# Kernel tuning notes

Measured on AMD Instinct MI355X. Metric: run time of the kernel, lower is better.

Reference implementation:

```python
import jax, jax.numpy as jnp
import numpy as np

DIM = 1024
HEADS = 16
HEAD_DIM = DIM // HEADS
MLP_HID = 4 * DIM
EPS = 1e-5


def layer_norm(x, g, b):
    mu = jnp.mean(x, axis=-1, keepdims=True)
    var = jnp.mean(jnp.square(x - mu), axis=-1, keepdims=True)
    return (x - mu) * jax.lax.rsqrt(var + EPS) * g + b


def setup_inputs() -> dict:
    key = jax.random.key(0)
    ks = jax.random.split(key, 8)
    s_in = 1.0 / np.sqrt(DIM)
    s_hid = 1.0 / np.sqrt(MLP_HID)
    return {
        "x": jax.random.normal(ks[0], (4, 2048, DIM), dtype=jnp.float32),
        "qkv_w": jax.random.uniform(ks[1], (3 * DIM, DIM), jnp.float32, -s_in, s_in),
        "proj_w": jax.random.uniform(ks[2], (DIM, DIM), jnp.float32, -s_in, s_in),
        "proj_b": jnp.zeros((DIM,), jnp.float32),
        "ln1_g": jnp.ones((DIM,), jnp.float32),
        "ln1_b": jnp.zeros((DIM,), jnp.float32),
        "w1": jax.random.uniform(ks[3], (MLP_HID, DIM), jnp.float32, -s_in, s_in),
        "b1": jnp.zeros((MLP_HID,), jnp.float32),
        "prelu_a": jnp.asarray(0.25, jnp.float32),
        "w2": jax.random.uniform(ks[4], (DIM, MLP_HID), jnp.float32, -s_hid, s_hid),
        "b2": jnp.zeros((DIM,), jnp.float32),
        "ln2_g": jnp.ones((DIM,), jnp.float32),
        "ln2_b": jnp.zeros((DIM,), jnp.float32),
    }


def reference(x, qkv_w, proj_w, proj_b, ln1_g, ln1_b, w1, b1, prelu_a, w2, b2, ln2_g, ln2_b):
    B, N, C = x.shape
    scale = HEAD_DIM ** (-0.5)

    # Multi-head self-attention (full NxN scores, softmax over keys)
    qkv = (x @ qkv_w.T).reshape(B, N, 3, HEADS, HEAD_DIM)
    qkv = jnp.transpose(qkv, (2, 0, 3, 1, 4))  # [3, B, H, N, hd]
    q, k, v = qkv[0] * scale, qkv[1], qkv[2]
    attn = jax.nn.softmax(jnp.einsum("bhnd,bhmd->bhnm", q, k), axis=-1)
    o = jnp.einsum("bhnm,bhmd->bhnd", attn, v)
    o = jnp.transpose(o, (0, 2, 1, 3)).reshape(B, N, C)
    o = o @ proj_w.T + proj_b

    # Post-norm residual 1
    x = layer_norm(x + o, ln1_g, ln1_b)

    # MLP: Linear -> (Dropout=identity in eval) -> PReLU -> Linear
    h = x @ w1.T + b1
    h = jnp.where(h >= 0, h, prelu_a * h)
    h = h @ w2.T + b2

    # Post-norm residual 2
    return layer_norm(x + h, ln2_g, ln2_b)
```

## Files before the change

kernel.cpp:

```cpp
#include <hip/hip_runtime.h>


typedef __attribute__((ext_vector_type(8))) short short8;
typedef __attribute__((ext_vector_type(4))) short short4v;
typedef __attribute__((ext_vector_type(4))) float floatx4;
typedef __attribute__((ext_vector_type(4))) int int4v;

__device__ __forceinline__ float bf2f(unsigned short u) {
    return __uint_as_float(((unsigned int)u) << 16);
}
__device__ __forceinline__ unsigned short f2bf(float f) {
    unsigned int u = __float_as_uint(f);
    u += 0x7FFFu + ((u >> 16) & 1u);
    return (unsigned short)(u >> 16);
}
__device__ __forceinline__ int pack2bf(float a, float b) {
    return (int)f2bf(a) | ((int)f2bf(b) << 16);
}
__device__ __forceinline__ unsigned int cvt_pk_bf16(float lo, float hi) {
    unsigned int r;
    asm("v_cvt_pk_bf16_f32 %0, %1, %2" : "=v"(r) : "v"(lo), "v"(hi));
    return r;
}

#define Q_PRESCALE 0.18033688011112043f

#if __has_builtin(__builtin_amdgcn_exp2f)
__device__ __forceinline__ float fast_exp2(float x) { return __builtin_amdgcn_exp2f(x); }
#else
__device__ __forceinline__ float fast_exp2(float x) { return __expf(x * 0.6931471805599453f); }
#endif

#if __has_builtin(__builtin_amdgcn_permlane32_swap) && __has_builtin(__builtin_amdgcn_permlane16_swap)
#define HAVE_PERMLANE 1
#else
#define HAVE_PERMLANE 0
#endif

__device__ __forceinline__ void async16(const unsigned short* g, unsigned short* l) {
    __builtin_amdgcn_global_load_lds(
        (const __attribute__((address_space(1))) unsigned int*)g,
        (__attribute__((address_space(3))) unsigned int*)l, 16, 0, 0);
}

#define BARRIER() do { __builtin_amdgcn_s_barrier(); asm volatile("" ::: "memory"); } while (0)
#define VMCNT(n)  asm volatile("s_waitcnt vmcnt(" #n ")" ::: "memory")

__global__ __launch_bounds__(256)
void cvt_f2b(const float* __restrict__ in, unsigned short* __restrict__ out) {
    const int i = (blockIdx.x * 256 + threadIdx.x) * 4;
    float4 v = *(const float4*)&in[i];
    short4v o;
    o[0] = (short)f2bf(v.x); o[1] = (short)f2bf(v.y);
    o[2] = (short)f2bf(v.z); o[3] = (short)f2bf(v.w);
    *(short4v*)&out[i] = o;
}

__global__ __launch_bounds__(512, 2)
void gemm256(const unsigned short* __restrict__ A,
             const unsigned short* __restrict__ W,
             const float* __restrict__ bias,
             const float* __restrict__ prelu,
             unsigned short* __restrict__ C,
             int N, int K, int qcols, int NNT) {
    __shared__ alignas(16) unsigned short lA[2][256 * 64];
    __shared__ alignas(16) unsigned short lB[2][256 * 64];

    const int nwg = gridDim.x;
    const int orig = blockIdx.x;
    const int q8 = nwg >> 3, r8 = nwg & 7, xx = orig & 7, rest = orig >> 3;
    const int wgid = (xx < r8 ? xx * (q8 + 1) : r8 * (q8 + 1) + (xx - r8) * q8) + rest;
    const int mt = wgid / NNT, nt = wgid % NNT;
    const int m0 = mt * 256, n0 = nt * 256;

    const int tid  = threadIdx.x;
    const int lane = tid & 63;
    const int wave = tid >> 6;
    const int lr = lane & 15, lq = lane >> 4;
    const int wrow = (wave >> 2) * 64;
    const int wcol = (wave & 3) * 32;
    const int srow = lane >> 3;
    const int scol = ((lane & 7) ^ srow) << 3;
    const int kx = lr & 7;

    const int NT = K >> 6;

    floatx4 acc[2][2][4][2] = {};
    short8 af[4][2], b0[2][2], b1[2][2];

    auto stA = [&](int d, int tt, int h) {
        #pragma unroll
        for (int it = 0; it < 2; ++it) {
            const int rb = h * 128 + (wave * 2 + it) * 8;
            async16(&A[(size_t)(m0 + rb + srow) * K + tt * 64 + scol], &lA[d][rb * 64]);
        }
    };
    auto stB = [&](int d, int tt, int h) {
        #pragma unroll
        for (int it = 0; it < 2; ++it) {
            const int rb = h * 128 + (wave * 2 + it) * 8;
            async16(&W[(size_t)(n0 + rb + srow) * K + tt * 64 + scol], &lB[d][rb * 64]);
        }
    };

#define RD_AF(dd, half)                                                        \
    _Pragma("unroll") for (int i = 0; i < 4; ++i)                              \
    _Pragma("unroll") for (int s = 0; s < 2; ++s)                              \
        af[i][s] = *(const short8*)&lA[dd][((half) * 128 + wrow + i * 16 + lr) * 64 + \
                                           (((s * 4 + lq) ^ kx) << 3)]
#define RD_B0(dd)                                                              \
    _Pragma("unroll") for (int j = 0; j < 2; ++j)                              \
    _Pragma("unroll") for (int s = 0; s < 2; ++s)                              \
        b0[j][s] = *(const short8*)&lB[dd][(wcol + j * 16 + lr) * 64 +         \
                                           (((s * 4 + lq) ^ kx) << 3)]
#define RD_B1(dd)                                                              \
    _Pragma("unroll") for (int j = 0; j < 2; ++j)                              \
    _Pragma("unroll") for (int s = 0; s < 2; ++s)                              \
        b1[j][s] = *(const short8*)&lB[dd][(128 + wcol + j * 16 + lr) * 64 +   \
                                           (((s * 4 + lq) ^ kx) << 3)]
#define MM256(mh, nh, BB)                                                      \
    _Pragma("unroll") for (int s = 0; s < 2; ++s)                              \
    _Pragma("unroll") for (int i = 0; i < 4; ++i)                              \
    _Pragma("unroll") for (int j = 0; j < 2; ++j)                              \
        acc[mh][nh][i][j] = __builtin_amdgcn_mfma_f32_16x16x32_bf16(           \
            af[i][s], BB[j][s], acc[mh][nh][i][j], 0, 0, 0)

    stA(0, 0, 0); stB(0, 0, 0); stB(0, 0, 1); stA(0, 0, 1);
    stA(1, 1, 0); stB(1, 1, 0); stB(1, 1, 1);
    VMCNT(6);
    BARRIER();
    RD_AF(0, 0);
    RD_B0(0);

    for (int t = 0; t < NT; ++t) {
        const int d = t & 1, e = d ^ 1;

        RD_B1(d);
        if (t + 1 < NT) stA(e, t + 1, 1);
        BARRIER();
        __builtin_amdgcn_s_setprio(1);
        MM256(0, 0, b0);
        __builtin_amdgcn_s_setprio(0);
        BARRIER();

        if (t + 2 < NT) stA(d, t + 2, 0);
        BARRIER();
        __builtin_amdgcn_s_setprio(1);
        MM256(0, 1, b1);
        __builtin_amdgcn_s_setprio(0);
        RD_AF(d, 1);
        BARRIER();

        if (t + 2 < NT) stB(d, t + 2, 0);
        BARRIER();
        __builtin_amdgcn_s_setprio(1);
        MM256(1, 1, b1);
        __builtin_amdgcn_s_setprio(0);
        if (t + 2 < NT)      { VMCNT(4); }
        else if (t + 1 < NT) { VMCNT(0); }
        BARRIER();

        if (t + 2 < NT) stB(d, t + 2, 1);
        BARRIER();
        __builtin_amdgcn_s_setprio(1);
        MM256(1, 0, b0);
        __builtin_amdgcn_s_setprio(0);
        if (t + 1 < NT) {
            RD_AF(e, 0);
            RD_B0(e);
        }
        BARRIER();
    }

#undef RD_AF
#undef RD_B0
#undef RD_B1
#undef MM256

    const bool hasb = (bias != nullptr);
    const bool hasp = (prelu != nullptr);
    const float slope = hasp ? prelu[0] : 0.f;
    #pragma unroll
    for (int mh = 0; mh < 2; ++mh)
        #pragma unroll
        for (int nh = 0; nh < 2; ++nh)
            #pragma unroll
            for (int j = 0; j < 2; ++j) {
                const int gc = n0 + nh * 128 + wcol + j * 16 + lr;
                const float bv = hasb ? bias[gc] : 0.f;
                const float cs = (gc < qcols) ? Q_PRESCALE : 1.f;
                #pragma unroll
                for (int i = 0; i < 4; ++i) {
                    const int gr = m0 + mh * 128 + wrow + i * 16 + lq * 4;
                    #pragma unroll
                    for (int r = 0; r < 4; ++r) {
                        float v = acc[mh][nh][i][j][r] + bv;
                        if (hasp && v < 0.f) v *= slope;
                        C[(size_t)(gr + r) * N + gc] = f2bf(v * cs);
                    }
                }
            }
}

__global__ __launch_bounds__(512, 2)
void gemm128(const unsigned short* __restrict__ A,
             const unsigned short* __restrict__ W,
             const float* __restrict__ bias,
             const float* __restrict__ prelu,
             unsigned short* __restrict__ C,
             int N, int K, int qcols, int NNT) {
    __shared__ alignas(16) unsigned short lA[2][128 * 64];
    __shared__ alignas(16) unsigned short lB[2][256 * 64];

    const int nwg = gridDim.x;
    const int orig = blockIdx.x;
    const int q8 = nwg >> 3, r8 = nwg & 7, xx = orig & 7, rest = orig >> 3;
    const int wgid = (xx < r8 ? xx * (q8 + 1) : r8 * (q8 + 1) + (xx - r8) * q8) + rest;
    const int mt = wgid / NNT, nt = wgid % NNT;
    const int m0 = mt * 128, n0 = nt * 256;

    const int tid  = threadIdx.x;
    const int lane = tid & 63;
    const int wave = tid >> 6;
    const int lr = lane & 15, lq = lane >> 4;
    const int wrow = (wave >> 2) * 64;
    const int wcol = (wave & 3) * 32;
    const int srow = lane >> 3;
    const int scol = ((lane & 7) ^ srow) << 3;
    const int kx = lr & 7;

    const int NT = K >> 6;

    floatx4 acc[2][4][2] = {};
    short8 af[4][2], b0[2][2], b1[2][2];

    auto stA = [&](int d, int tt) {
        #pragma unroll
        for (int it = 0; it < 2; ++it) {
            const int rb = (wave * 2 + it) * 8;
            async16(&A[(size_t)(m0 + rb + srow) * K + tt * 64 + scol], &lA[d][rb * 64]);
        }
    };
    auto stB = [&](int d, int tt, int h) {
        #pragma unroll
        for (int it = 0; it < 2; ++it) {
            const int rb = (wave * 2 + it) * 8;
            async16(&W[(size_t)(n0 + h * 128 + rb + srow) * K + tt * 64 + scol],
                    &lB[d][(h * 128 + rb) * 64]);
        }
    };

#define RD_AF(dd)                                                              \
    _Pragma("unroll") for (int i = 0; i < 4; ++i)                              \
    _Pragma("unroll") for (int s = 0; s < 2; ++s)                              \
        af[i][s] = *(const short8*)&lA[dd][(wrow + i * 16 + lr) * 64 +         \
                                           (((s * 4 + lq) ^ kx) << 3)]
#define RD_B0(dd)                                                              \
    _Pragma("unroll") for (int j = 0; j < 2; ++j)                              \
    _Pragma("unroll") for (int s = 0; s < 2; ++s)                              \
        b0[j][s] = *(const short8*)&lB[dd][(wcol + j * 16 + lr) * 64 +         \
                                           (((s * 4 + lq) ^ kx) << 3)]
#define RD_B1(dd)                                                              \
    _Pragma("unroll") for (int j = 0; j < 2; ++j)                              \
    _Pragma("unroll") for (int s = 0; s < 2; ++s)                              \
        b1[j][s] = *(const short8*)&lB[dd][(128 + wcol + j * 16 + lr) * 64 +   \
                                           (((s * 4 + lq) ^ kx) << 3)]
#define MM128(nh, BB)                                                          \
    _Pragma("unroll") for (int s = 0; s < 2; ++s)                              \
    _Pragma("unroll") for (int i = 0; i < 4; ++i)                              \
    _Pragma("unroll") for (int j = 0; j < 2; ++j)                              \
        acc[nh][i][j] = __builtin_amdgcn_mfma_f32_16x16x32_bf16(               \
            af[i][s], BB[j][s], acc[nh][i][j], 0, 0, 0)

    stA(0, 0); stB(0, 0, 0); stB(0, 0, 1);
    stA(1, 1); stB(1, 1, 0);
    VMCNT(4);
    BARRIER();
    RD_AF(0);
    RD_B0(0);

    for (int t = 0; t < NT; ++t) {
        const int d = t & 1, e = d ^ 1;

        RD_B1(d);
        if (t + 1 < NT) stB(e, t + 1, 1);
        BARRIER();
        __builtin_amdgcn_s_setprio(1);
        MM128(0, b0);
        __builtin_amdgcn_s_setprio(0);
        if (t + 1 < NT) { VMCNT(2); }
        BARRIER();

        if (t + 2 < NT) { stA(d, t + 2); stB(d, t + 2, 0); }
        BARRIER();
        __builtin_amdgcn_s_setprio(1);
        MM128(1, b1);
        __builtin_amdgcn_s_setprio(0);
        if (t + 2 < NT)      { VMCNT(4); }
        else if (t + 1 < NT) { VMCNT(0); }
        if (t + 1 < NT) {
            RD_AF(e);
            RD_B0(e);
        }
        BARRIER();
    }

#undef RD_AF
#undef RD_B0
#undef RD_B1
#undef MM128

    const bool hasb = (bias != nullptr);
    const bool hasp = (prelu != nullptr);
    const float slope = hasp ? prelu[0] : 0.f;
    #pragma unroll
    for (int nh = 0; nh < 2; ++nh)
        #pragma unroll
        for (int j = 0; j < 2; ++j) {
            const int gc = n0 + nh * 128 + wcol + j * 16 + lr;
            const float bv = hasb ? bias[gc] : 0.f;
            const float cs = (gc < qcols) ? Q_PRESCALE : 1.f;
            #pragma unroll
            for (int i = 0; i < 4; ++i) {
                const int gr = m0 + wrow + i * 16 + lq * 4;
                #pragma unroll
                for (int r = 0; r < 4; ++r) {
                    float v = acc[nh][i][j][r] + bv;
                    if (hasp && v < 0.f) v *= slope;
                    C[(size_t)(gr + r) * N + gc] = f2bf(v * cs);
                }
            }
        }
}

__global__ __launch_bounds__(256)
void transpose_v(const unsigned short* __restrict__ qkv,
                 unsigned short* __restrict__ vt) {
    const int kt = blockIdx.x;
    const int bh = blockIdx.y;
    const int b = bh >> 4, h = bh & 15;
    __shared__ unsigned short tile[64 * 65];
    for (int t = threadIdx.x; t < 512; t += 256) {
        const int key = t >> 3, c8 = (t & 7) << 3;
        short8 v8 = *(const short8*)&qkv[((size_t)(b * 2048 + kt * 64 + key)) * 3072 +
                                         2048 + h * 64 + c8];
        #pragma unroll
        for (int e = 0; e < 8; ++e)
            tile[key * 65 + c8 + e] = (unsigned short)v8[e];
    }
    __syncthreads();
    for (int t = threadIdx.x; t < 512; t += 256) {
        const int d = t >> 3, k8 = (t & 7) << 3;
        short8 o;
        #pragma unroll
        for (int e = 0; e < 8; ++e)
            o[e] = (short)tile[(k8 + e) * 65 + d];
        *(short8*)&vt[((size_t)bh * 64 + d) * 2048 + kt * 64 + k8] = o;
    }
}

__global__ __launch_bounds__(256, 2)
void attn_kernel(const unsigned short* __restrict__ qkv,
                 const unsigned short* __restrict__ vt,
                 unsigned short* __restrict__ o_attn) {
    const int id = blockIdx.x;
    const int qg = id >> 6;
    const int bh = id & 63;
    const int b = bh >> 4, h = bh & 15;
    const int tid  = threadIdx.x;
    const int lane = tid & 63;
    const int wave = tid >> 6;
    const int lr = lane & 15;
    const int lq = lane >> 4;
    const int q0 = (qg * 4 + wave) * 64;
    const size_t row0 = (size_t)(b * 2048) * 3072;

    __shared__ alignas(16) unsigned short lK[2][64 * 64];
    __shared__ alignas(16) unsigned short lV[2][64 * 64];

    short8 qf[4][2];
    #pragma unroll
    for (int j = 0; j < 4; ++j)
        #pragma unroll
        for (int s = 0; s < 2; ++s)
            qf[j][s] = *(const short8*)&qkv[row0 + (size_t)(q0 + j * 16 + lr) * 3072 +
                                            h * 64 + s * 32 + lq * 8];

    floatx4 oacc[4][4] = {};
    float l_i[4] = {0.f, 0.f, 0.f, 0.f};

    const int srow = lane >> 3;
    const int scol = (((lane & 7) ^ srow)) << 3;
    const int kx = lr & 7;

    auto stage = [&](int bi, int kc) {
        #pragma unroll
        for (int it2 = 0; it2 < 2; ++it2) {
            const int it = wave * 2 + it2;
            const int row = it * 8 + srow;
            async16(&qkv[row0 + (size_t)(kc + row) * 3072 + 1024 + h * 64 + scol],
                    &lK[bi][it * 512 + lane * 8]);
            async16(&vt[((size_t)bh * 64 + row) * 2048 + kc + scol],
                    &lV[bi][it * 512 + lane * 8]);
        }
    };

    asm volatile("s_waitcnt vmcnt(0)" ::: "memory");
    stage(0, 0);

    #pragma unroll 1
    for (int c = 0; c < 32; ++c) {
        const int cur = c & 1;
        if (c + 1 < 32) {
            stage(cur ^ 1, (c + 1) * 64);
            asm volatile("s_waitcnt vmcnt(4)" ::: "memory");
        } else {
            asm volatile("s_waitcnt vmcnt(0)" ::: "memory");
        }
        __builtin_amdgcn_s_barrier();
        asm volatile("" ::: "memory");

        floatx4 sacc[4][4] = {};
        #pragma unroll
        for (int s = 0; s < 2; ++s) {
            short8 kf[4];
            #pragma unroll
            for (int i = 0; i < 4; ++i) {
                const int r = i * 16 + lr;
                kf[i] = *(const short8*)&lK[cur][r * 64 + (((s * 4 + lq) ^ kx) << 3)];
            }
            #pragma unroll
            for (int i = 0; i < 4; ++i)
                #pragma unroll
                for (int j = 0; j < 4; ++j)
                    sacc[i][j] = __builtin_amdgcn_mfma_f32_16x16x32_bf16(
                        kf[i], qf[j][s], sacc[i][j], 0, 0, 0);
        }

        unsigned int pkd[4][4][2];
        #pragma unroll
        for (int i = 0; i < 4; ++i)
            #pragma unroll
            for (int j = 0; j < 4; ++j) {
                const float e0 = fast_exp2(sacc[i][j][0]);
                const float e1 = fast_exp2(sacc[i][j][1]);
                const float e2 = fast_exp2(sacc[i][j][2]);
                const float e3 = fast_exp2(sacc[i][j][3]);
                l_i[j] += (e0 + e1) + (e2 + e3);
                pkd[i][j][0] = cvt_pk_bf16(e0, e1);
                pkd[i][j][1] = cvt_pk_bf16(e2, e3);
            }

        #pragma unroll
        for (int s = 0; s < 2; ++s) {
            short8 vf[4];
            #pragma unroll
            for (int i = 0; i < 4; ++i) {
                const int r = i * 16 + lr;
                vf[i] = *(const short8*)&lV[cur][r * 64 + (((s * 4 + lq) ^ kx) << 3)];
            }
            short8 bq[4];
            #pragma unroll
            for (int j = 0; j < 4; ++j) {
                int4v iv;
#if HAVE_PERMLANE
                auto p0 = __builtin_amdgcn_permlane32_swap(
                    pkd[2 * s][j][0], pkd[2 * s + 1][j][0], false, false);
                auto w0 = __builtin_amdgcn_permlane16_swap(p0[0], p0[1], false, false);
                auto p1 = __builtin_amdgcn_permlane32_swap(
                    pkd[2 * s][j][1], pkd[2 * s + 1][j][1], false, false);
                auto w1 = __builtin_amdgcn_permlane16_swap(p1[0], p1[1], false, false);
                iv[0] = (int)w0[0]; iv[1] = (int)w1[0];
                iv[2] = (int)w0[1]; iv[3] = (int)w1[1];
#else
                const int src0 = lr + ((lq & 1) * 2) * 16;
                const int src1 = src0 + 16;
                const bool hi = (lq >> 1) != 0;
                int a0 = __shfl((int)pkd[2 * s][j][0], src0, 64);
                int c0 = __shfl((int)pkd[2 * s + 1][j][0], src0, 64);
                int a1 = __shfl((int)pkd[2 * s][j][1], src0, 64);
                int c1 = __shfl((int)pkd[2 * s + 1][j][1], src0, 64);
                int a2 = __shfl((int)pkd[2 * s][j][0], src1, 64);
                int c2 = __shfl((int)pkd[2 * s + 1][j][0], src1, 64);
                int a3 = __shfl((int)pkd[2 * s][j][1], src1, 64);
                int c3 = __shfl((int)pkd[2 * s + 1][j][1], src1, 64);
                iv[0] = hi ? c0 : a0;
                iv[1] = hi ? c1 : a1;
                iv[2] = hi ? c2 : a2;
                iv[3] = hi ? c3 : a3;
#endif
                bq[j] = __builtin_bit_cast(short8, iv);
            }
            #pragma unroll
            for (int j = 0; j < 4; ++j)
                #pragma unroll
                for (int i = 0; i < 4; ++i)
                    oacc[i][j] = __builtin_amdgcn_mfma_f32_16x16x32_bf16(
                        vf[i], bq[j], oacc[i][j], 0, 0, 0);
        }

        asm volatile("s_waitcnt lgkmcnt(0)" ::: "memory");
        __builtin_amdgcn_s_barrier();
        asm volatile("" ::: "memory");
    }

    #pragma unroll
    for (int j = 0; j < 4; ++j) {
        l_i[j] += __shfl_xor(l_i[j], 16, 64);
        l_i[j] += __shfl_xor(l_i[j], 32, 64);
        const float rl = 1.f / l_i[j];
        const int q = q0 + j * 16 + lr;
        #pragma unroll
        for (int i = 0; i < 4; ++i) {
            int2 pk;
            pk.x = pack2bf(oacc[i][j][0] * rl, oacc[i][j][1] * rl);
            pk.y = pack2bf(oacc[i][j][2] * rl, oacc[i][j][3] * rl);
            *(int2*)&o_attn[((size_t)(b * 2048 + q)) * 1024 + h * 64 + i * 16 + lq * 4] = pk;
        }
    }
}

__global__ __launch_bounds__(256)
void ln_f32_bf16(const float* __restrict__ x,
                 const unsigned short* __restrict__ res,
                 const float* __restrict__ g,
                 const float* __restrict__ bta,
                 unsigned short* __restrict__ out) {
    const int row = blockIdx.x;
    const int t = threadIdx.x;
    const size_t base = (size_t)row * 1024;

    float4 xv = *(const float4*)&x[base + t * 4];
    short4v rv = *(const short4v*)&res[base + t * 4];
    float v[4] = { xv.x + bf2f((unsigned short)rv[0]),
                   xv.y + bf2f((unsigned short)rv[1]),
                   xv.z + bf2f((unsigned short)rv[2]),
                   xv.w + bf2f((unsigned short)rv[3]) };
    float s = 0.f, s2 = 0.f;
    #pragma unroll
    for (int k = 0; k < 4; ++k) { s += v[k]; s2 += v[k] * v[k]; }
    #pragma unroll
    for (int off = 32; off > 0; off >>= 1) {
        s  += __shfl_xor(s, off, 64);
        s2 += __shfl_xor(s2, off, 64);
    }
    __shared__ float red[8];
    const int wave = t >> 6;
    if ((t & 63) == 0) { red[wave] = s; red[4 + wave] = s2; }
    __syncthreads();
    s  = red[0] + red[1] + red[2] + red[3];
    s2 = red[4] + red[5] + red[6] + red[7];
    const float mean = s * (1.f / 1024.f);
    const float var  = fmaxf(s2 * (1.f / 1024.f) - mean * mean, 0.f);
    const float inv  = rsqrtf(var + 1e-5f);

    short4v ov;
    #pragma unroll
    for (int k = 0; k < 4; ++k) {
        int c = t * 4 + k;
        ov[k] = (short)f2bf((v[k] - mean) * inv * g[c] + bta[c]);
    }
    *(short4v*)&out[base + t * 4] = ov;
}

__global__ __launch_bounds__(256)
void ln_bf16_f32(const unsigned short* __restrict__ x,
                 const unsigned short* __restrict__ res,
                 const float* __restrict__ g,
                 const float* __restrict__ bta,
                 float* __restrict__ out) {
    const int row = blockIdx.x;
    const int t = threadIdx.x;
    const size_t base = (size_t)row * 1024;

    short4v xv = *(const short4v*)&x[base + t * 4];
    short4v rv = *(const short4v*)&res[base + t * 4];
    float v[4];
    float s = 0.f, s2 = 0.f;
    #pragma unroll
    for (int k = 0; k < 4; ++k) {
        v[k] = bf2f((unsigned short)xv[k]) + bf2f((unsigned short)rv[k]);
        s += v[k];
        s2 += v[k] * v[k];
    }
    #pragma unroll
    for (int off = 32; off > 0; off >>= 1) {
        s  += __shfl_xor(s, off, 64);
        s2 += __shfl_xor(s2, off, 64);
    }
    __shared__ float red[8];
    const int wave = t >> 6;
    if ((t & 63) == 0) { red[wave] = s; red[4 + wave] = s2; }
    __syncthreads();
    s  = red[0] + red[1] + red[2] + red[3];
    s2 = red[4] + red[5] + red[6] + red[7];
    const float mean = s * (1.f / 1024.f);
    const float var  = fmaxf(s2 * (1.f / 1024.f) - mean * mean, 0.f);
    const float inv  = rsqrtf(var + 1e-5f);

    float4 ov;
    ov.x = (v[0] - mean) * inv * g[t * 4 + 0] + bta[t * 4 + 0];
    ov.y = (v[1] - mean) * inv * g[t * 4 + 1] + bta[t * 4 + 1];
    ov.z = (v[2] - mean) * inv * g[t * 4 + 2] + bta[t * 4 + 2];
    ov.w = (v[3] - mean) * inv * g[t * 4 + 3] + bta[t * 4 + 3];
    *(float4*)&out[base + t * 4] = ov;
}

extern "C" void kernel_launch(void* const* d_in, const int* in_sizes, int n_in,
                              void* d_out, int out_size, void* d_ws, size_t ws_size,
                              hipStream_t stream) {
    const float* x      = (const float*)d_in[0];
    const float* qkv_w  = (const float*)d_in[1];
    const float* proj_w = (const float*)d_in[2];
    const float* proj_b = (const float*)d_in[3];
    const float* ln1_g  = (const float*)d_in[4];
    const float* ln1_b  = (const float*)d_in[5];
    const float* w1     = (const float*)d_in[6];
    const float* b1     = (const float*)d_in[7];
    const float* prelu  = (const float*)d_in[8];
    const float* w2     = (const float*)d_in[9];
    const float* b2     = (const float*)d_in[10];
    const float* ln2_g  = (const float*)d_in[11];
    const float* ln2_b  = (const float*)d_in[12];
    float* out = (float*)d_out;

    char* ws = (char*)d_ws;
    const size_t MB = 1024 * 1024;
    unsigned short* wqkvb  = (unsigned short*)(ws);
    unsigned short* wprojb = (unsigned short*)(ws + 6 * MB);
    unsigned short* w1b    = (unsigned short*)(ws + 8 * MB);
    unsigned short* w2b    = (unsigned short*)(ws + 16 * MB);
    unsigned short* xb     = (unsigned short*)(ws + 24 * MB);
    unsigned short* vtb    = (unsigned short*)(ws + 24 * MB);
    unsigned short* qkvb   = (unsigned short*)(ws + 40 * MB);
    unsigned short* oat    = (unsigned short*)(ws + 88 * MB);
    unsigned short* pout   = (unsigned short*)(ws + 24 * MB);
    unsigned short* x1b    = (unsigned short*)(ws + 40 * MB);
    unsigned short* h1     = (unsigned short*)(ws + 56 * MB);
    unsigned short* h2     = (unsigned short*)(ws + 24 * MB);

    cvt_f2b<<<8192, 256, 0, stream>>>(x,      xb);
    cvt_f2b<<<3072, 256, 0, stream>>>(qkv_w,  wqkvb);
    cvt_f2b<<<1024, 256, 0, stream>>>(proj_w, wprojb);
    cvt_f2b<<<4096, 256, 0, stream>>>(w1,     w1b);
    cvt_f2b<<<4096, 256, 0, stream>>>(w2,     w2b);

    gemm128<<<dim3(64 * 12), 512, 0, stream>>>(xb, wqkvb, nullptr, nullptr,
                                               qkvb, 3072, 1024, 1024, 12);
    transpose_v<<<dim3(32, 64), 256, 0, stream>>>(qkvb, vtb);
    attn_kernel<<<512, 256, 0, stream>>>(qkvb, vtb, oat);
    gemm128<<<dim3(64 * 4), 512, 0, stream>>>(oat, wprojb, proj_b, nullptr,
                                              pout, 1024, 1024, 0, 4);
    ln_f32_bf16<<<8192, 256, 0, stream>>>(x, pout, ln1_g, ln1_b, x1b);
    gemm256<<<dim3(32 * 16), 512, 0, stream>>>(x1b, w1b, b1, prelu,
                                               h1, 4096, 1024, 0, 16);
    gemm128<<<dim3(64 * 4), 512, 0, stream>>>(h1, w2b, b2, nullptr,
                                              h2, 1024, 4096, 0, 4);
    ln_bf16_f32<<<8192, 256, 0, stream>>>(x1b, h2, ln2_g, ln2_b, out);
}
```

Baseline: 506.0 us.

## Merge weight conversions, unroll GEMM loops by two, reschedule gemm128 LDS reads

The four weight fp32->bf16 conversion launches become one kernel that writes into the contiguous workspace. Both GEMM main loops are unrolled by two with compile-time buffer indices. gemm128 now issues its LDS fragment reads right before each MFMA half and waits on lgkmcnt, instead of prefetching the next tile's fragments. The attention MFMA blocks are also wrapped in s_setprio. Moving the reads later trades prefetch overlap for lower register pressure, and the unrolled loop assumes an even number of K tiles.

```diff
diff --git a/kernel.cpp b/kernel.cpp
--- a/kernel.cpp
+++ b/kernel.cpp
@@ -45,6 +45,7 @@
 
 #define BARRIER() do { __builtin_amdgcn_s_barrier(); asm volatile("" ::: "memory"); } while (0)
 #define VMCNT(n)  asm volatile("s_waitcnt vmcnt(" #n ")" ::: "memory")
+#define LGKM0()   asm volatile("s_waitcnt lgkmcnt(0)" ::: "memory")
 
 __global__ __launch_bounds__(256)
 void cvt_f2b(const float* __restrict__ in, unsigned short* __restrict__ out) {
@@ -54,6 +55,26 @@
     o[0] = (short)f2bf(v.x); o[1] = (short)f2bf(v.y);
     o[2] = (short)f2bf(v.z); o[3] = (short)f2bf(v.w);
     *(short4v*)&out[i] = o;
+}
+
+__global__ __launch_bounds__(256)
+void cvt_weights(const float* __restrict__ qkv_w, const float* __restrict__ proj_w,
+                 const float* __restrict__ w1, const float* __restrict__ w2,
+                 unsigned short* __restrict__ dst) {
+    const int b = blockIdx.x;
+    const float* src;
+    int off;
+    if (b < 3072)      { src = qkv_w;  off = b; }
+    else if (b < 4096) { src = proj_w; off = b - 3072; }
+    else if (b < 8192) { src = w1;     off = b - 4096; }
+    else               { src = w2;     off = b - 8192; }
+    const size_t si = (size_t)off * 1024 + threadIdx.x * 4;
+    const size_t di = (size_t)b   * 1024 + threadIdx.x * 4;
+    float4 v = *(const float4*)&src[si];
+    short4v o;
+    o[0] = (short)f2bf(v.x); o[1] = (short)f2bf(v.y);
+    o[2] = (short)f2bf(v.z); o[3] = (short)f2bf(v.w);
+    *(short4v*)&dst[di] = o;
 }
 
 __global__ __launch_bounds__(512, 2)
@@ -132,9 +153,7 @@
     RD_AF(0, 0);
     RD_B0(0);
 
-    for (int t = 0; t < NT; ++t) {
-        const int d = t & 1, e = d ^ 1;
-
+    auto tile = [&](int t, int d, int e) {
         RD_B1(d);
         if (t + 1 < NT) stA(e, t + 1, 1);
         BARRIER();
@@ -170,6 +189,11 @@
             RD_B0(e);
         }
         BARRIER();
+    };
+
+    for (int t = 0; t < NT; t += 2) {
+        tile(t, 0, 1);
+        tile(t + 1, 1, 0);
     }
 
 #undef RD_AF
@@ -276,33 +300,33 @@
     stA(1, 1); stB(1, 1, 0);
     VMCNT(4);
     BARRIER();
-    RD_AF(0);
-    RD_B0(0);
-
-    for (int t = 0; t < NT; ++t) {
-        const int d = t & 1, e = d ^ 1;
-
-        RD_B1(d);
+
+    auto tile = [&](int t, int d, int e) {
+        RD_AF(d);
+        RD_B0(d);
         if (t + 1 < NT) stB(e, t + 1, 1);
         BARRIER();
+        LGKM0();
         __builtin_amdgcn_s_setprio(1);
         MM128(0, b0);
         __builtin_amdgcn_s_setprio(0);
-        if (t + 1 < NT) { VMCNT(2); }
-        BARRIER();
-
+        BARRIER();
+
+        RD_B1(d);
         if (t + 2 < NT) { stA(d, t + 2); stB(d, t + 2, 0); }
         BARRIER();
+        LGKM0();
         __builtin_amdgcn_s_setprio(1);
         MM128(1, b1);
         __builtin_amdgcn_s_setprio(0);
         if (t + 2 < NT)      { VMCNT(4); }
         else if (t + 1 < NT) { VMCNT(0); }
-        if (t + 1 < NT) {
-            RD_AF(e);
-            RD_B0(e);
-        }
-        BARRIER();
+        BARRIER();
+    };
+
+    for (int t = 0; t < NT; t += 2) {
+        tile(t, 0, 1);
+        tile(t + 1, 1, 0);
     }
 
 #undef RD_AF
@@ -429,12 +453,14 @@
                 const int r = i * 16 + lr;
                 kf[i] = *(const short8*)&lK[cur][r * 64 + (((s * 4 + lq) ^ kx) << 3)];
             }
+            __builtin_amdgcn_s_setprio(1);
             #pragma unroll
             for (int i = 0; i < 4; ++i)
                 #pragma unroll
                 for (int j = 0; j < 4; ++j)
                     sacc[i][j] = __builtin_amdgcn_mfma_f32_16x16x32_bf16(
                         kf[i], qf[j][s], sacc[i][j], 0, 0, 0);
+            __builtin_amdgcn_s_setprio(0);
         }
 
         unsigned int pkd[4][4][2];
@@ -491,12 +517,14 @@
 #endif
                 bq[j] = __builtin_bit_cast(short8, iv);
             }
+            __builtin_amdgcn_s_setprio(1);
             #pragma unroll
             for (int j = 0; j < 4; ++j)
                 #pragma unroll
                 for (int i = 0; i < 4; ++i)
                     oacc[i][j] = __builtin_amdgcn_mfma_f32_16x16x32_bf16(
                         vf[i], bq[j], oacc[i][j], 0, 0, 0);
+            __builtin_amdgcn_s_setprio(0);
         }
 
         asm volatile("s_waitcnt lgkmcnt(0)" ::: "memory");
@@ -639,11 +667,9 @@
     unsigned short* h1     = (unsigned short*)(ws + 56 * MB);
     unsigned short* h2     = (unsigned short*)(ws + 24 * MB);
 
-    cvt_f2b<<<8192, 256, 0, stream>>>(x,      xb);
-    cvt_f2b<<<3072, 256, 0, stream>>>(qkv_w,  wqkvb);
-    cvt_f2b<<<1024, 256, 0, stream>>>(proj_w, wprojb);
-    cvt_f2b<<<4096, 256, 0, stream>>>(w1,     w1b);
-    cvt_f2b<<<4096, 256, 0, stream>>>(w2,     w2b);
+    cvt_f2b<<<8192, 256, 0, stream>>>(x, xb);
+    cvt_weights<<<12288, 256, 0, stream>>>(qkv_w, proj_w, w1, w2,
+                                           (unsigned short*)ws);
 
     gemm128<<<dim3(64 * 12), 512, 0, stream>>>(xb, wqkvb, nullptr, nullptr,
                                                qkvb, 3072, 1024, 1024, 12);
```

After: 488.7 us. 3.4% less time.
